# Kernel optimization log

Measured on AMD Instinct MI355X. Metric: run time of the kernel, lower is better.

The kernel has to match this reference:

```python
import jax, jax.numpy as jnp
import numpy as np

DIM = 512
HEADS = 4
DH = 128          # dim_head
CHUNK = 16        # chunk_size
MAX_LR = 0.01     # default_adaptive_step_transform max_lr
EPS = 1e-6        # flax RMSNorm epsilon


def setup_inputs() -> dict:
    key = jax.random.key(0)
    ks = jax.random.split(key, 8)
    B, S = 2, 2048
    dim_inner = HEADS * DH
    seq = jax.random.normal(ks[0], (B, S, DIM), jnp.float32)
    store_norm_scale = jnp.ones((DIM,), jnp.float32)               # RMSNorm scale
    W_kv = (jax.random.normal(ks[1], (DIM, 2 * dim_inner)) * 0.02).astype(jnp.float32)
    W_step = (jax.random.normal(ks[2], (DIM, HEADS)) * 0.02).astype(jnp.float32)
    W_mom = (jax.random.normal(ks[3], (DIM, HEADS)) * 0.02).astype(jnp.float32)
    W_decay = (jax.random.normal(ks[4], (DIM, HEADS)) * 0.02).astype(jnp.float32)
    # past memory-MLP weights, shared init expanded to (b, h, dh, dh)
    w0 = jnp.broadcast_to((jax.random.normal(ks[5], (DH, DH)) * 0.02).astype(jnp.float32), (B, HEADS, DH, DH)) + 0.0
    w1 = jnp.broadcast_to((jax.random.normal(ks[6], (DH, DH)) * 0.02).astype(jnp.float32), (B, HEADS, DH, DH)) + 0.0
    return {"seq": seq, "store_norm_scale": store_norm_scale, "W_kv": W_kv,
            "W_step": W_step, "W_mom": W_mom, "W_decay": W_decay, "w0": w0, "w1": w1}


def _mlp(w0, w1, x):
    # MemoryMLP depth=2: x @ w0 ; silu ; @ w1
    return jax.nn.silu(x @ w0) @ w1


def _chunk_loss(w0, w1, k, lr, v):
    pred = _mlp(w0, w1, k)                       # [c, d]
    return jnp.sum(jnp.mean((pred - v) ** 2, axis=-1) * lr)


def _binop(e1, e2):
    a1, b1 = e1
    a2, b2 = e2
    return a1 * a2, a2 * b1 + b2


def _lin_scan(a, b):
    # first-order linear recurrence y_t = a_t * y_{t-1} + b_t along chunk axis (axis=2)
    return jax.lax.associative_scan(_binop, (a, b), axis=2)[1]


def _store(seq, store_norm_scale, W_kv, W_step, W_mom, W_decay, w0, w1):
    B, S, _ = seq.shape
    n = S // CHUNK
    # pre RMSNorm (with scale)
    x = seq * jax.lax.rsqrt(jnp.mean(seq * seq, axis=-1, keepdims=True) + EPS) * store_norm_scale
    # adaptive per-token lr:  sigmoid(x @ W_step) * max_lr  -> [b, h, s]
    lr = jax.nn.sigmoid(jnp.einsum('bsd,dh->bhs', x, W_step)) * MAX_LR
    # per-chunk mean -> momentum / decay factors  [b, h, n, 1]
    mean = x.reshape(B, n, CHUNK, DIM).mean(axis=2)
    mom = jax.nn.sigmoid(jnp.einsum('bnd,dh->bhn', mean, W_mom))[..., None]
    dec = jax.nn.sigmoid(jnp.einsum('bnd,dh->bhn', mean, W_decay))[..., None]
    # keys / values  [b*h, n, c, dh]
    kv = x @ W_kv
    k, v = jnp.split(kv, 2, axis=-1)
    k = k.reshape(B, n, CHUNK, HEADS, DH).transpose(0, 3, 1, 2, 4).reshape(B * HEADS, n, CHUNK, DH)
    v = v.reshape(B, n, CHUNK, HEADS, DH).transpose(0, 3, 1, 2, 4).reshape(B * HEADS, n, CHUNK, DH)
    lr_ch = lr.reshape(B, HEADS, n, CHUNK).reshape(B * HEADS, n, CHUNK)
    w0bh = w0.reshape(B * HEADS, DH, DH)
    w1bh = w1.reshape(B * HEADS, DH, DH)
    # per-chunk gradients of the MLP loss at the *past* weights (all chunks independent)
    gfn = jax.grad(_chunk_loss, argnums=(0, 1))
    gfn = jax.vmap(gfn, in_axes=(None, None, 0, 0, 0))   # over chunks n
    gfn = jax.vmap(gfn, in_axes=(0, 0, 0, 0, 0))         # over b*h
    g0, g1 = gfn(w0bh, w1bh, k, lr_ch, v)                # [b*h, n, dh, dh]
    s0 = (-g0).reshape(B, HEADS, n, DH * DH)             # surprises
    s1 = (-g1).reshape(B, HEADS, n, DH * DH)
    # momentum scan then decay scan (Titans update rule)
    m0 = _lin_scan(jnp.broadcast_to(mom, s0.shape), s0)
    m1 = _lin_scan(jnp.broadcast_to(mom, s1.shape), s1)
    u0 = _lin_scan(jnp.broadcast_to(1.0 - dec, m0.shape), m0)
    u1 = _lin_scan(jnp.broadcast_to(1.0 - dec, m1.shape), m1)
    updates = jnp.stack([u0.reshape(B, HEADS, n, DH, DH),
                         u1.reshape(B, HEADS, n, DH, DH)], axis=0)  # [2, b, h, n, dh, dh]
    return updates


def reference(seq, store_norm_scale, W_kv, W_step, W_mom, W_decay, w0, w1):
    return _store(seq, store_norm_scale, W_kv, W_step, W_mom, W_decay, w0, w1)
```

## Files before the change

### kernel.cpp

```cpp
#include <hip/hip_runtime.h>

#define DIMX 512
#define HEADSX 4
#define DHX 128
#define CHX 16
#define NCX 128
#define SX 2048
#define BX 2
#define BHX 8
#define PADX 520
#define PADF 136

typedef unsigned short ushort_t;
typedef unsigned int uint_t;
typedef short bf16x8 __attribute__((ext_vector_type(8)));
typedef float f32x4 __attribute__((ext_vector_type(4)));

__device__ __forceinline__ float sigmoidf_(float z){ return 1.0f/(1.0f + __expf(-z)); }

__device__ __forceinline__ ushort_t f2bf(float f){
  uint_t u = __float_as_uint(f);
  return (ushort_t)((u + 0x7FFFu + ((u >> 16) & 1u)) >> 16);
}
__device__ __forceinline__ uint_t pk2(float a, float b){
  return (uint_t)f2bf(a) | ((uint_t)f2bf(b) << 16);
}

#define AS1 __attribute__((address_space(1)))
#define AS3 __attribute__((address_space(3)))
__device__ __forceinline__ void gl_lds16(const void* g, void* l){
#if __has_builtin(__builtin_amdgcn_global_load_lds)
  __builtin_amdgcn_global_load_lds((const AS1 void*)g, (AS3 void*)l, 16, 0, 0);
#else
  *(uint4*)l = *(const uint4*)g;
#endif
}

__global__ __launch_bounds__(256) void k_rms_lr(const float* __restrict__ seq,
    const float* __restrict__ scale, const float* __restrict__ Wstep,
    float* __restrict__ x, float* __restrict__ lrArr){
  int tok = blockIdx.x; int tid = threadIdx.x;
  const float* row = seq + (size_t)tok*DIMX;
  float v0 = row[tid], v1 = row[tid+256];
  float ss = v0*v0 + v1*v1;
  #pragma unroll
  for (int o=32;o>0;o>>=1) ss += __shfl_down(ss,o,64);
  __shared__ float red[4];
  __shared__ float rs_s;
  int wv = tid>>6, ln = tid&63;
  if (ln==0) red[wv]=ss;
  __syncthreads();
  if (tid==0){
    float ms = (red[0]+red[1]+red[2]+red[3]) * (1.0f/DIMX);
    rs_s = 1.0f/sqrtf(ms + 1e-6f);
  }
  __syncthreads();
  float rs = rs_s;
  float x0 = v0*rs*scale[tid];
  float x1 = v1*rs*scale[tid+256];
  size_t xo = (size_t)tok*DIMX;
  x[xo+tid]=x0; x[xo+tid+256]=x1;
  float a0 = x0*Wstep[tid*4+0] + x1*Wstep[(tid+256)*4+0];
  float a1 = x0*Wstep[tid*4+1] + x1*Wstep[(tid+256)*4+1];
  float a2 = x0*Wstep[tid*4+2] + x1*Wstep[(tid+256)*4+2];
  float a3 = x0*Wstep[tid*4+3] + x1*Wstep[(tid+256)*4+3];
  #pragma unroll
  for (int o=32;o>0;o>>=1){
    a0 += __shfl_down(a0,o,64); a1 += __shfl_down(a1,o,64);
    a2 += __shfl_down(a2,o,64); a3 += __shfl_down(a3,o,64);
  }
  __shared__ float red4[4][4];
  if (ln==0){ red4[wv][0]=a0; red4[wv][1]=a1; red4[wv][2]=a2; red4[wv][3]=a3; }
  __syncthreads();
  if (tid<4){
    float d = red4[0][tid]+red4[1][tid]+red4[2][tid]+red4[3][tid];
    int b = tok>>11, s = tok&2047;
    lrArr[(size_t)(b*HEADSX+tid)*SX + s] = 0.01f * sigmoidf_(d);
  }
}

__global__ __launch_bounds__(64) void k_stats(const float* __restrict__ x,
    const float* __restrict__ Wmom, const float* __restrict__ Wdec,
    float* __restrict__ momw, float* __restrict__ decw){
  int blk = blockIdx.x; int b = blk>>7, nc = blk&127; int ln = threadIdx.x;
  float am[4]={0,0,0,0}, ad[4]={0,0,0,0};
  const float* base = x + ((size_t)(b*SX + nc*CHX))*DIMX;
  for (int r=0;r<8;r++){
    int d = ln + 64*r;
    float m = 0.0f;
    #pragma unroll
    for (int c=0;c<CHX;c++) m += base[(size_t)c*DIMX + d];
    m *= (1.0f/CHX);
    #pragma unroll
    for (int h=0;h<4;h++){ am[h]+=m*Wmom[d*4+h]; ad[h]+=m*Wdec[d*4+h]; }
  }
  #pragma unroll
  for (int h=0;h<4;h++){
    #pragma unroll
    for (int o=32;o>0;o>>=1){ am[h]+=__shfl_down(am[h],o,64); ad[h]+=__shfl_down(ad[h],o,64); }
  }
  if (ln==0){
    #pragma unroll
    for (int h=0;h<4;h++){
      momw[(b*HEADSX+h)*NCX + nc] = sigmoidf_(am[h]);
      decw[(b*HEADSX+h)*NCX + nc] = 1.0f - sigmoidf_(ad[h]);
    }
  }
}

__global__ __launch_bounds__(256) void k_prep(const float* __restrict__ Wkv,
    const float* __restrict__ w0, const float* __restrict__ w1,
    ushort_t* __restrict__ WkvT, ushort_t* __restrict__ w0T,
    ushort_t* __restrict__ w1T, ushort_t* __restrict__ w1n){
  int blk = blockIdx.x; int tid = threadIdx.x;
  if (blk < 64){
    int h = blk >> 4, kt = blk & 15;
    for (int i=tid; i<8192; i+=256){
      int kk = i >> 8, col = i & 255;
      int wcol = (col < 128) ? (h*128 + col) : (384 + h*128 + col);
      float v = Wkv[(size_t)(kt*32+kk)*1024 + wcol];
      WkvT[(((size_t)h*16 + kt)*256 + col)*32 + kk] = f2bf(v);
    }
  } else {
    int bh = blk - 64;
    size_t base = (size_t)bh*16384;
    for (int i=tid; i<16384; i+=256){
      int r = i >> 7, c = i & 127;
      w0T[base + i] = f2bf(w0[base + (size_t)c*128 + r]);
      w1T[base + i] = f2bf(w1[base + (size_t)c*128 + r]);
      w1n[base + i] = f2bf(w1[base + i]);
    }
  }
}

__global__ __launch_bounds__(256) void k_fused(const float* __restrict__ x,
    const ushort_t* __restrict__ WkvT, const ushort_t* __restrict__ w0T,
    const ushort_t* __restrict__ w1T, const ushort_t* __restrict__ w1n,
    const float* __restrict__ lrArr,
    ushort_t* __restrict__ fac0, ushort_t* __restrict__ fac1){
  int blk = blockIdx.x;
  int bh = blk & 7, t = blk >> 3;
  int b = bh >> 2, h = bh & 3;
  int bt = bh*NCX + t;
  __shared__ __align__(16) ushort_t xs[16*PADX];
  __shared__ __align__(16) ushort_t ks[16*PADF];
  __shared__ __align__(16) ushort_t as_[16*PADF];
  __shared__ __align__(16) ushort_t dp_[16*PADF];
  __shared__ __align__(16) ushort_t dh_[16*PADF];
  int tid = threadIdx.x;
  int wv = tid>>6, lane = tid&63;
  int quad = lane>>4, nl = lane&15;
  const f32x4 zero = {0.f,0.f,0.f,0.f};

  const float* xb = x + ((size_t)(b*SX + t*CHX))*DIMX;
  #pragma unroll
  for (int it=0; it<8; it++){
    int f = tid + 256*it;
    int c = f >> 7, k4 = f & 127;
    float4 q = ((const float4*)xb)[(size_t)c*128 + k4];
    uint2 u; u.x = pk2(q.x,q.y); u.y = pk2(q.z,q.w);
    *(uint2*)&xs[c*PADX + k4*4] = u;
  }
  __syncthreads();

  f32x4 kacc[2] = {zero, zero};
  f32x4 vacc[2] = {zero, zero};
  const ushort_t* wkvh = WkvT + (size_t)h*16*256*32;
  for (int kt=0; kt<16; kt++){
    bf16x8 Af = *(const bf16x8*)&xs[nl*PADX + kt*32 + quad*8];
    #pragma unroll
    for (int s=0; s<2; s++){
      int ktile = 2*wv + s;
      bf16x8 Bk = *(const bf16x8*)&wkvh[((size_t)kt*256 + (ktile*16+nl))*32 + quad*8];
      kacc[s] = __builtin_amdgcn_mfma_f32_16x16x32_bf16(Af, Bk, kacc[s], 0,0,0);
      int vtile = 8 + 2*wv + s;
      bf16x8 Bv = *(const bf16x8*)&wkvh[((size_t)kt*256 + (vtile*16+nl))*32 + quad*8];
      vacc[s] = __builtin_amdgcn_mfma_f32_16x16x32_bf16(Af, Bv, vacc[s], 0,0,0);
    }
  }
  #pragma unroll
  for (int s=0;s<2;s++){
    #pragma unroll
    for (int r=0;r<4;r++)
      ks[(quad*4+r)*PADF + 32*wv + 16*s + nl] = f2bf(kacc[s][r]);
  }
  __syncthreads();

  const ushort_t* w0b = w0T + (size_t)bh*16384;
  f32x4 hacc[2] = {zero, zero};
  for (int kt=0; kt<4; kt++){
    bf16x8 Af = *(const bf16x8*)&ks[nl*PADF + kt*32 + quad*8];
    #pragma unroll
    for (int s=0; s<2; s++){
      int n0 = (2*wv+s)*16;
      bf16x8 Bf = *(const bf16x8*)&w0b[(size_t)(n0+nl)*128 + kt*32 + quad*8];
      hacc[s] = __builtin_amdgcn_mfma_f32_16x16x32_bf16(Af, Bf, hacc[s], 0,0,0);
    }
  }
  float sp[2][4];
  #pragma unroll
  for (int s=0;s<2;s++){
    #pragma unroll
    for (int r=0;r<4;r++){
      float hh = hacc[s][r];
      float sg = sigmoidf_(hh);
      float a  = hh*sg;
      sp[s][r] = sg*(1.0f + hh*(1.0f-sg));
      as_[(quad*4+r)*PADF + 32*wv + 16*s + nl] = f2bf(a);
    }
  }
  __syncthreads();

  const ushort_t* w1tb = w1T + (size_t)bh*16384;
  f32x4 pacc[2] = {zero, zero};
  for (int kt=0; kt<4; kt++){
    bf16x8 Af = *(const bf16x8*)&as_[nl*PADF + kt*32 + quad*8];
    #pragma unroll
    for (int s=0; s<2; s++){
      int n0 = (2*wv+s)*16;
      bf16x8 Bf = *(const bf16x8*)&w1tb[(size_t)(n0+nl)*128 + kt*32 + quad*8];
      pacc[s] = __builtin_amdgcn_mfma_f32_16x16x32_bf16(Af, Bf, pacc[s], 0,0,0);
    }
  }
  float lrv[4];
  #pragma unroll
  for (int r=0;r<4;r++) lrv[r] = lrArr[(size_t)bh*SX + t*CHX + quad*4 + r];
  #pragma unroll
  for (int s=0;s<2;s++){
    #pragma unroll
    for (int r=0;r<4;r++){
      float dp = (2.0f/DHX)*lrv[r]*(pacc[s][r] - vacc[s][r]);
      dp_[(quad*4+r)*PADF + 32*wv + 16*s + nl] = f2bf(dp);
    }
  }
  __syncthreads();

  const ushort_t* w1nb = w1n + (size_t)bh*16384;
  f32x4 dacc[2] = {zero, zero};
  for (int kt=0; kt<4; kt++){
    bf16x8 Af = *(const bf16x8*)&dp_[nl*PADF + kt*32 + quad*8];
    #pragma unroll
    for (int s=0; s<2; s++){
      int n0 = (2*wv+s)*16;
      bf16x8 Bf = *(const bf16x8*)&w1nb[(size_t)(n0+nl)*128 + kt*32 + quad*8];
      dacc[s] = __builtin_amdgcn_mfma_f32_16x16x32_bf16(Af, Bf, dacc[s], 0,0,0);
    }
  }
  #pragma unroll
  for (int s=0;s<2;s++){
    #pragma unroll
    for (int r=0;r<4;r++)
      dh_[(quad*4+r)*PADF + 32*wv + 16*s + nl] = f2bf(dacc[s][r]*sp[s][r]);
  }
  __syncthreads();

  {
    int p = tid & 127, which = tid >> 7;
    const ushort_t* s0 = which ? dh_ : ks;
    const ushort_t* s1 = which ? dp_ : as_;
    ushort_t rowv[32];
    #pragma unroll
    for (int c=0;c<16;c++){ rowv[c] = s0[c*PADF + p]; rowv[16+c] = s1[c*PADF + p]; }
    ushort_t* dst = (which ? fac1 : fac0) + ((size_t)bt*128 + p)*32;
    const uint4* rv = (const uint4*)rowv;
    uint4* dq = (uint4*)dst;
    dq[0]=rv[0]; dq[1]=rv[1]; dq[2]=rv[2]; dq[3]=rv[3];
  }
}

__global__ __launch_bounds__(128) void k_scan(const ushort_t* __restrict__ fac0,
    const ushort_t* __restrict__ fac1,
    const float* __restrict__ momw, const float* __restrict__ decw,
    float* __restrict__ out){
  int blk = blockIdx.x;
  int bh = blk & 7; int rest = blk >> 3;
  int ig = rest >> 3, jb = rest & 7;
  int i0 = ig*16, j0 = jb*16;
  int tid = threadIdx.x;
  int wv = tid >> 6, lane = tid & 63;
  int quad = lane >> 4, rrow = lane & 15;
  __shared__ __align__(16) ushort_t sbuf[2][1024];
  const ushort_t* gsl = (wv==0)
      ? fac0 + ((size_t)bh*NCX*128 + (size_t)i0)*32
      : fac1 + ((size_t)bh*NCX*128 + (size_t)j0)*32;

  f32x4 m_ = {0.f,0.f,0.f,0.f};
  f32x4 u_ = {0.f,0.f,0.f,0.f};
  const f32x4 zero = {0.f,0.f,0.f,0.f};
  size_t obase = ((size_t)(wv*BHX + bh)*NCX)*((size_t)DHX*DHX) + (size_t)i0*DHX + j0;
  const float* mop = momw + bh*NCX;
  const float* dep = decw + bh*NCX;

  gl_lds16((const void*)(gsl + (size_t)lane*8), (void*)&sbuf[0][wv*512]);
  __syncthreads();
  int b = 0;
  for (int t=0; t<NCX; t++){
    if (t+1 < NCX)
      gl_lds16((const void*)(gsl + (size_t)(t+1)*4096 + (size_t)lane*8),
               (void*)&sbuf[b^1][wv*512]);
    float mo = mop[t], de = dep[t];
    bf16x8 fa = {0,0,0,0,0,0,0,0};
    bf16x8 fb = {0,0,0,0,0,0,0,0};
    if (quad < 2){
      fa = *(const bf16x8*)&sbuf[b][      rrow*32 + wv*16 + quad*8];
      fb = *(const bf16x8*)&sbuf[b][512 + rrow*32 + wv*16 + quad*8];
    }
    f32x4 g = __builtin_amdgcn_mfma_f32_16x16x32_bf16(fa, fb, zero, 0, 0, 0);
    size_t ob = obase + (size_t)t*(DHX*DHX);
    #pragma unroll
    for (int r=0;r<4;r++){
      m_[r] = mo*m_[r] - g[r];
      u_[r] = de*u_[r] + m_[r];
      out[ob + (size_t)(quad*4+r)*DHX + rrow] = u_[r];
    }
    __syncthreads();
    b ^= 1;
  }
}

extern "C" void kernel_launch(void* const* d_in, const int* in_sizes, int n_in,
                              void* d_out, int out_size, void* d_ws, size_t ws_size,
                              hipStream_t stream) {
  (void)in_sizes; (void)n_in; (void)out_size; (void)ws_size;
  const float* seq   = (const float*)d_in[0];
  const float* scale = (const float*)d_in[1];
  const float* Wkv   = (const float*)d_in[2];
  const float* Wstep = (const float*)d_in[3];
  const float* Wmom  = (const float*)d_in[4];
  const float* Wdec  = (const float*)d_in[5];
  const float* w0    = (const float*)d_in[6];
  const float* w1    = (const float*)d_in[7];
  float* out = (float*)d_out;
  float* ws  = (float*)d_ws;

  float*    x     = ws;
  ushort_t* fac0  = (ushort_t*)(ws + 2097152);
  ushort_t* fac1  = (ushort_t*)(ws + 4194304);
  ushort_t* WkvT  = (ushort_t*)(ws + 6291456);
  ushort_t* w0T   = (ushort_t*)(ws + 6553600);
  ushort_t* w1T   = (ushort_t*)(ws + 6619136);
  ushort_t* w1n   = (ushort_t*)(ws + 6684672);
  float*    lrArr = ws + 6750208;
  float*    momw  = ws + 6766592;
  float*    decw  = ws + 6767616;

  k_prep<<<dim3(72), dim3(256), 0, stream>>>(Wkv, w0, w1, WkvT, w0T, w1T, w1n);
  k_rms_lr<<<dim3(BX*SX), dim3(256), 0, stream>>>(seq, scale, Wstep, x, lrArr);
  k_stats<<<dim3(BX*NCX), dim3(64), 0, stream>>>(x, Wmom, Wdec, momw, decw);
  k_fused<<<dim3(BHX*NCX), dim3(256), 0, stream>>>(x, WkvT, w0T, w1T, w1n, lrArr, fac0, fac1);
  k_scan<<<dim3(512), dim3(128), 0, stream>>>(fac0, fac1, momw, decw, out);
}
```

Measured before the change: 255.0 us.

## Split sequential chunk scan into segmented three-pass scan with carry propagation

Replaces the single sequential scan over all 128 chunks (512 blocks) with a three-phase segmented scan. The first pass computes per-segment local momentum/decay sums, a small kernel propagates carries across the 8 segments, and a fix pass recomputes each segment from its carry-in and writes the output. This exposes more parallelism (4096 blocks instead of 512). In exchange it recomputes the MFMA outer products twice, adds launches and carry traffic, and falls back to the old kernel if the workspace is too small.

```diff
diff --git a/kernel.cpp b/kernel.cpp
--- a/kernel.cpp
+++ b/kernel.cpp
@@ -10,6 +10,8 @@
 #define BHX 8
 #define PADX 520
 #define PADF 136
+#define NSEG 8
+#define SEGL 16
 
 typedef unsigned short ushort_t;
 typedef unsigned int uint_t;
@@ -318,10 +320,157 @@
   }
 }
 
+__global__ __launch_bounds__(128, 8) void k_scan_sum(const ushort_t* __restrict__ fac0,
+    const ushort_t* __restrict__ fac1,
+    const float* __restrict__ momw, const float* __restrict__ decw,
+    float* __restrict__ carry){
+  int blk = blockIdx.x;
+  int bh = blk & 7;
+  int rest = blk >> 3;
+  int sg = rest % 7;
+  int tile = rest / 7;
+  int ig = tile >> 3, jb = tile & 7;
+  int i0 = ig*16, j0 = jb*16;
+  int tid = threadIdx.x;
+  int wv = tid >> 6, lane = tid & 63;
+  int quad = lane >> 4, rrow = lane & 15;
+  __shared__ __align__(16) ushort_t sbuf[2][1024];
+  const ushort_t* gsl = (wv==0)
+      ? fac0 + (((size_t)bh*NCX + sg*SEGL)*128 + (size_t)i0)*32
+      : fac1 + (((size_t)bh*NCX + sg*SEGL)*128 + (size_t)j0)*32;
+
+  f32x4 m_ = {0.f,0.f,0.f,0.f};
+  f32x4 u_ = {0.f,0.f,0.f,0.f};
+  const f32x4 zero = {0.f,0.f,0.f,0.f};
+  const float* mop = momw + bh*NCX + sg*SEGL;
+  const float* dep = decw + bh*NCX + sg*SEGL;
+
+  gl_lds16((const void*)(gsl + (size_t)lane*8), (void*)&sbuf[0][wv*512]);
+  __syncthreads();
+  int b = 0;
+  for (int t=0; t<SEGL; t++){
+    if (t+1 < SEGL)
+      gl_lds16((const void*)(gsl + (size_t)(t+1)*4096 + (size_t)lane*8),
+               (void*)&sbuf[b^1][wv*512]);
+    float mo = mop[t], de = dep[t];
+    bf16x8 fa = {0,0,0,0,0,0,0,0};
+    bf16x8 fb = {0,0,0,0,0,0,0,0};
+    if (quad < 2){
+      fa = *(const bf16x8*)&sbuf[b][      rrow*32 + wv*16 + quad*8];
+      fb = *(const bf16x8*)&sbuf[b][512 + rrow*32 + wv*16 + quad*8];
+    }
+    f32x4 g = __builtin_amdgcn_mfma_f32_16x16x32_bf16(fa, fb, zero, 0, 0, 0);
+    #pragma unroll
+    for (int r=0;r<4;r++){
+      m_[r] = mo*m_[r] - g[r];
+      u_[r] = de*u_[r] + m_[r];
+    }
+    __syncthreads();
+    b ^= 1;
+  }
+  size_t base = ((((size_t)wv*8 + bh)*64 + tile)*8 + sg)*512;
+  #pragma unroll
+  for (int r=0;r<4;r++){
+    carry[base +       r*64 + lane] = m_[r];
+    carry[base + 256 + r*64 + lane] = u_[r];
+  }
+}
+
+__global__ __launch_bounds__(256) void k_scan_carry(const float* __restrict__ momw,
+    const float* __restrict__ decw, float* __restrict__ carry){
+  int blk = blockIdx.x;
+  int bh = (blk >> 6) & 7;
+  int j = threadIdx.x;
+  size_t base = (size_t)blk * 4096;
+  const float* mop = momw + bh*NCX;
+  const float* dep = decw + bh*NCX;
+  float m = 0.f, u = 0.f;
+  for (int sg=0; sg<NSEG; sg++){
+    float gm = 0.f, gu = 0.f;
+    if (sg < NSEG-1){
+      gm = carry[base + (size_t)sg*512 + j];
+      gu = carry[base + (size_t)sg*512 + 256 + j];
+    }
+    carry[base + (size_t)sg*512 + j]       = m;
+    carry[base + (size_t)sg*512 + 256 + j] = u;
+    if (sg < NSEG-1){
+      float A = 1.f, C = 0.f, D = 1.f;
+      #pragma unroll
+      for (int t=0; t<SEGL; t++){
+        float mo = mop[sg*SEGL + t], de = dep[sg*SEGL + t];
+        A = mo*A;
+        C = de*C + A;
+        D = de*D;
+      }
+      float nm = A*m + gm;
+      u = C*m + D*u + gu;
+      m = nm;
+    }
+  }
+}
+
+__global__ __launch_bounds__(128, 8) void k_scan_fix(const ushort_t* __restrict__ fac0,
+    const ushort_t* __restrict__ fac1,
+    const float* __restrict__ momw, const float* __restrict__ decw,
+    const float* __restrict__ carry, float* __restrict__ out){
+  int blk = blockIdx.x;
+  int bh = blk & 7;
+  int sg = (blk >> 3) & 7;
+  int tile = blk >> 6;
+  int ig = tile >> 3, jb = tile & 7;
+  int i0 = ig*16, j0 = jb*16;
+  int tid = threadIdx.x;
+  int wv = tid >> 6, lane = tid & 63;
+  int quad = lane >> 4, rrow = lane & 15;
+  __shared__ __align__(16) ushort_t sbuf[2][1024];
+  const ushort_t* gsl = (wv==0)
+      ? fac0 + (((size_t)bh*NCX + sg*SEGL)*128 + (size_t)i0)*32
+      : fac1 + (((size_t)bh*NCX + sg*SEGL)*128 + (size_t)j0)*32;
+
+  f32x4 m_, u_;
+  size_t cb = ((((size_t)wv*8 + bh)*64 + tile)*8 + sg)*512;
+  #pragma unroll
+  for (int r=0;r<4;r++){
+    m_[r] = carry[cb +       r*64 + lane];
+    u_[r] = carry[cb + 256 + r*64 + lane];
+  }
+  const f32x4 zero = {0.f,0.f,0.f,0.f};
+  size_t obase = (((size_t)(wv*BHX + bh)*NCX) + sg*SEGL)*((size_t)DHX*DHX)
+               + (size_t)i0*DHX + j0;
+  const float* mop = momw + bh*NCX + sg*SEGL;
+  const float* dep = decw + bh*NCX + sg*SEGL;
+
+  gl_lds16((const void*)(gsl + (size_t)lane*8), (void*)&sbuf[0][wv*512]);
+  __syncthreads();
+  int b = 0;
+  for (int t=0; t<SEGL; t++){
+    if (t+1 < SEGL)
+      gl_lds16((const void*)(gsl + (size_t)(t+1)*4096 + (size_t)lane*8),
+               (void*)&sbuf[b^1][wv*512]);
+    float mo = mop[t], de = dep[t];
+    bf16x8 fa = {0,0,0,0,0,0,0,0};
+    bf16x8 fb = {0,0,0,0,0,0,0,0};
+    if (quad < 2){
+      fa = *(const bf16x8*)&sbuf[b][      rrow*32 + wv*16 + quad*8];
+      fb = *(const bf16x8*)&sbuf[b][512 + rrow*32 + wv*16 + quad*8];
+    }
+    f32x4 g = __builtin_amdgcn_mfma_f32_16x16x32_bf16(fa, fb, zero, 0, 0, 0);
+    size_t ob = obase + (size_t)t*(DHX*DHX);
+    #pragma unroll
+    for (int r=0;r<4;r++){
+      m_[r] = mo*m_[r] - g[r];
+      u_[r] = de*u_[r] + m_[r];
+      out[ob + (size_t)(quad*4+r)*DHX + rrow] = u_[r];
+    }
+    __syncthreads();
+    b ^= 1;
+  }
+}
+
 extern "C" void kernel_launch(void* const* d_in, const int* in_sizes, int n_in,
                               void* d_out, int out_size, void* d_ws, size_t ws_size,
                               hipStream_t stream) {
-  (void)in_sizes; (void)n_in; (void)out_size; (void)ws_size;
+  (void)in_sizes; (void)n_in; (void)out_size;
   const float* seq   = (const float*)d_in[0];
   const float* scale = (const float*)d_in[1];
   const float* Wkv   = (const float*)d_in[2];
@@ -343,10 +492,19 @@
   float*    lrArr = ws + 6750208;
   float*    momw  = ws + 6766592;
   float*    decw  = ws + 6767616;
+  float*    carry = ws + 6768640;
+  const size_t need_bytes = (size_t)(6768640 + 4194304) * sizeof(float);
 
   k_prep<<<dim3(72), dim3(256), 0, stream>>>(Wkv, w0, w1, WkvT, w0T, w1T, w1n);
   k_rms_lr<<<dim3(BX*SX), dim3(256), 0, stream>>>(seq, scale, Wstep, x, lrArr);
   k_stats<<<dim3(BX*NCX), dim3(64), 0, stream>>>(x, Wmom, Wdec, momw, decw);
   k_fused<<<dim3(BHX*NCX), dim3(256), 0, stream>>>(x, WkvT, w0T, w1T, w1n, lrArr, fac0, fac1);
-  k_scan<<<dim3(512), dim3(128), 0, stream>>>(fac0, fac1, momw, decw, out);
-}
+
+  if (ws_size >= need_bytes) {
+    k_scan_sum<<<dim3(8*7*64), dim3(128), 0, stream>>>(fac0, fac1, momw, decw, carry);
+    k_scan_carry<<<dim3(1024), dim3(256), 0, stream>>>(momw, decw, carry);
+    k_scan_fix<<<dim3(8*8*64), dim3(128), 0, stream>>>(fac0, fac1, momw, decw, carry, out);
+  } else {
+    k_scan<<<dim3(512), dim3(128), 0, stream>>>(fac0, fac1, momw, decw, out);
+  }
+}
```

After: 316.9 us. +24.3%, slower.

## Split scan into single-wave blocks with register prefetch, transpose Wkv via LDS

Applied to the files above, without the earlier changes.

The scan kernel now launches 1024 single-wave blocks, one per weight matrix and 16x16 tile, where before it used 512 two-wave blocks. The old path staged factor rows in LDS with global_load_lds, a double buffer and a barrier every step. The new kernel loads the bf16 fragments straight into registers, prefetches two time steps ahead and processes two steps per iteration, so there are no barriers. This should add parallelism and remove synchronisation in the output-write-bound scan. k_prep also transposes Wkv through a shared tile so the global stores are coalesced.

```diff
diff --git a/kernel.cpp b/kernel.cpp
--- a/kernel.cpp
+++ b/kernel.cpp
@@ -26,16 +26,6 @@
   return (uint_t)f2bf(a) | ((uint_t)f2bf(b) << 16);
 }
 
-#define AS1 __attribute__((address_space(1)))
-#define AS3 __attribute__((address_space(3)))
-__device__ __forceinline__ void gl_lds16(const void* g, void* l){
-#if __has_builtin(__builtin_amdgcn_global_load_lds)
-  __builtin_amdgcn_global_load_lds((const AS1 void*)g, (AS3 void*)l, 16, 0, 0);
-#else
-  *(uint4*)l = *(const uint4*)g;
-#endif
-}
-
 __global__ __launch_bounds__(256) void k_rms_lr(const float* __restrict__ seq,
     const float* __restrict__ scale, const float* __restrict__ Wstep,
     float* __restrict__ x, float* __restrict__ lrArr){
@@ -115,11 +105,17 @@
   int blk = blockIdx.x; int tid = threadIdx.x;
   if (blk < 64){
     int h = blk >> 4, kt = blk & 15;
+    __shared__ ushort_t tile[256][33];
     for (int i=tid; i<8192; i+=256){
       int kk = i >> 8, col = i & 255;
       int wcol = (col < 128) ? (h*128 + col) : (384 + h*128 + col);
       float v = Wkv[(size_t)(kt*32+kk)*1024 + wcol];
-      WkvT[(((size_t)h*16 + kt)*256 + col)*32 + kk] = f2bf(v);
+      tile[col][kk] = f2bf(v);
+    }
+    __syncthreads();
+    for (int i=tid; i<8192; i+=256){
+      int col = i >> 5, kk = i & 31;
+      WkvT[(((size_t)h*16 + kt)*256 + col)*32 + kk] = tile[col][kk];
     }
   } else {
     int bh = blk - 64;
@@ -268,53 +264,66 @@
   }
 }
 
-__global__ __launch_bounds__(128) void k_scan(const ushort_t* __restrict__ fac0,
+__global__ __launch_bounds__(64) void k_scan3(const ushort_t* __restrict__ fac0,
     const ushort_t* __restrict__ fac1,
     const float* __restrict__ momw, const float* __restrict__ decw,
     float* __restrict__ out){
   int blk = blockIdx.x;
-  int bh = blk & 7; int rest = blk >> 3;
-  int ig = rest >> 3, jb = rest & 7;
-  int i0 = ig*16, j0 = jb*16;
-  int tid = threadIdx.x;
-  int wv = tid >> 6, lane = tid & 63;
+  int bh  = blk & 7;
+  int jb  = (blk >> 3) & 7;
+  int ig  = (blk >> 6) & 7;
+  int mat = blk >> 9;
+  int lane = threadIdx.x;
   int quad = lane >> 4, rrow = lane & 15;
-  __shared__ __align__(16) ushort_t sbuf[2][1024];
-  const ushort_t* gsl = (wv==0)
-      ? fac0 + ((size_t)bh*NCX*128 + (size_t)i0)*32
-      : fac1 + ((size_t)bh*NCX*128 + (size_t)j0)*32;
-
-  f32x4 m_ = {0.f,0.f,0.f,0.f};
-  f32x4 u_ = {0.f,0.f,0.f,0.f};
   const f32x4 zero = {0.f,0.f,0.f,0.f};
-  size_t obase = ((size_t)(wv*BHX + bh)*NCX)*((size_t)DHX*DHX) + (size_t)i0*DHX + j0;
+  const bf16x8 fz = {0,0,0,0,0,0,0,0};
+
+  size_t rowbase = (size_t)bh*NCX*128;
+  const ushort_t* pa = fac0 + (rowbase + (size_t)(ig*16 + rrow))*32 + mat*16 + quad*8;
+  const ushort_t* pb = fac1 + (rowbase + (size_t)(jb*16 + rrow))*32 + mat*16 + quad*8;
+  bool act = (quad < 2);
+
+  bf16x8 fa0=fz, fb0=fz, fa1=fz, fb1=fz;
+  if (act){
+    fa0 = *(const bf16x8*)(pa);
+    fb0 = *(const bf16x8*)(pb);
+    fa1 = *(const bf16x8*)(pa + 4096);
+    fb1 = *(const bf16x8*)(pb + 4096);
+  }
+
+  f32x4 m_ = zero, u_ = zero;
+  size_t obase = ((size_t)(mat*BHX + bh)*NCX)*((size_t)DHX*DHX)
+               + (size_t)(ig*16 + quad*4)*DHX + (size_t)(jb*16 + rrow);
   const float* mop = momw + bh*NCX;
   const float* dep = decw + bh*NCX;
 
-  gl_lds16((const void*)(gsl + (size_t)lane*8), (void*)&sbuf[0][wv*512]);
-  __syncthreads();
-  int b = 0;
-  for (int t=0; t<NCX; t++){
-    if (t+1 < NCX)
-      gl_lds16((const void*)(gsl + (size_t)(t+1)*4096 + (size_t)lane*8),
-               (void*)&sbuf[b^1][wv*512]);
+  for (int t=0; t<NCX; t+=2){
+    bf16x8 na0=fz, nb0=fz, na1=fz, nb1=fz;
+    if (act && (t+2 < NCX)){
+      na0 = *(const bf16x8*)(pa + (size_t)(t+2)*4096);
+      nb0 = *(const bf16x8*)(pb + (size_t)(t+2)*4096);
+      na1 = *(const bf16x8*)(pa + (size_t)(t+3)*4096);
+      nb1 = *(const bf16x8*)(pb + (size_t)(t+3)*4096);
+    }
     float mo = mop[t], de = dep[t];
-    bf16x8 fa = {0,0,0,0,0,0,0,0};
-    bf16x8 fb = {0,0,0,0,0,0,0,0};
-    if (quad < 2){
-      fa = *(const bf16x8*)&sbuf[b][      rrow*32 + wv*16 + quad*8];
-      fb = *(const bf16x8*)&sbuf[b][512 + rrow*32 + wv*16 + quad*8];
-    }
-    f32x4 g = __builtin_amdgcn_mfma_f32_16x16x32_bf16(fa, fb, zero, 0, 0, 0);
-    size_t ob = obase + (size_t)t*(DHX*DHX);
+    f32x4 g = __builtin_amdgcn_mfma_f32_16x16x32_bf16(fa0, fb0, zero, 0,0,0);
+    float* ob = out + obase + (size_t)t*(DHX*DHX);
     #pragma unroll
     for (int r=0;r<4;r++){
       m_[r] = mo*m_[r] - g[r];
       u_[r] = de*u_[r] + m_[r];
-      out[ob + (size_t)(quad*4+r)*DHX + rrow] = u_[r];
-    }
-    __syncthreads();
-    b ^= 1;
+      ob[(size_t)r*DHX] = u_[r];
+    }
+    mo = mop[t+1]; de = dep[t+1];
+    g = __builtin_amdgcn_mfma_f32_16x16x32_bf16(fa1, fb1, zero, 0,0,0);
+    ob += (size_t)DHX*DHX;
+    #pragma unroll
+    for (int r=0;r<4;r++){
+      m_[r] = mo*m_[r] - g[r];
+      u_[r] = de*u_[r] + m_[r];
+      ob[(size_t)r*DHX] = u_[r];
+    }
+    fa0=na0; fb0=nb0; fa1=na1; fb1=nb1;
   }
 }
 
@@ -348,5 +357,5 @@
   k_rms_lr<<<dim3(BX*SX), dim3(256), 0, stream>>>(seq, scale, Wstep, x, lrArr);
   k_stats<<<dim3(BX*NCX), dim3(64), 0, stream>>>(x, Wmom, Wdec, momw, decw);
   k_fused<<<dim3(BHX*NCX), dim3(256), 0, stream>>>(x, WkvT, w0T, w1T, w1n, lrArr, fac0, fac1);
-  k_scan<<<dim3(512), dim3(128), 0, stream>>>(fac0, fac1, momw, decw, out);
-}
+  k_scan3<<<dim3(1024), dim3(64), 0, stream>>>(fac0, fac1, momw, decw, out);
+}
```

Measured after the change: 246.3 us. 3.4% less time.
